# Optimization experiments

Measured on AMD Instinct MI355X. Metric: run time of the kernel, lower is better.

The kernel has to match this reference:

```python
import jax, jax.numpy as jnp
import numpy as np

B, D, R = 256, 4096, 8
MAX_R = 2 * R - 1  # static upper bound on radius (torch uses data-dependent max)


def setup_inputs() -> dict:
    key = jax.random.key(0)
    ks = jax.random.split(key, 6)
    x = jax.random.randint(ks[0], (B, D), 0, 2).astype(jnp.float32)  # binary spins
    W = jax.random.normal(ks[1], (D, D), jnp.float32) / np.float32(np.sqrt(D))
    b = jax.random.normal(ks[2], (D,), jnp.float32)
    radius_raw = jax.random.randint(ks[3], (B, 1), 0, MAX_R)  # +1 in reference -> [1, 2R-1]
    gumbel_u = jax.random.uniform(ks[4], (B, D), jnp.float32)
    u = jax.random.uniform(ks[5], (B,), jnp.float32)
    return {"x": x, "W": W, "b": b, "radius_raw": radius_raw, "gumbel_u": gumbel_u, "u": u}


def _model(x, W, b):
    # quadratic pseudo-Boolean energy model: per-sample scalar score
    return 0.5 * jnp.einsum('bi,ij,bj->b', x, W, x) + x @ b


def reference(x, W, b, radius_raw, gumbel_u, u):
    radius = radius_raw + 1                                   # [B,1] in [1, 2R-1]
    r_mask = (jnp.arange(MAX_R)[None, :] < radius).astype(x.dtype)  # [B, MAX_R]

    score_x = _model(x, W, b)                                 # [B]
    grad = jax.lax.stop_gradient(
        jax.grad(lambda xx: _model(xx, W, b).sum())(x))       # [B,D], detached

    delta_x = -(2.0 * x - 1.0)
    score_change_x = delta_x * grad / 2.0                     # logits of proposal

    # multinomial without replacement == Gumbel top-k on the logits
    eps = 1e-10
    g = -jnp.log(-jnp.log(jnp.clip(gumbel_u, eps, 1.0 - eps)))
    _, indices = jax.lax.top_k(score_change_x + g, MAX_R)     # [B, MAX_R]

    rows = jnp.arange(B)[:, None]
    cur_bits = x[rows, indices]                               # gather
    new_bits = 1.0 - cur_bits
    y = x.at[rows, indices].set(r_mask * new_bits + (1.0 - r_mask) * cur_bits)

    delta_y = -(2.0 * y - 1.0)
    score_y = _model(y, W, b)
    score_change_y = delta_y * grad / 2.0

    log_pypx = score_y - score_x
    log_tilde_pxpy = -jnp.sum(grad * (y - x), axis=-1)
    log_zxzy = (jax.scipy.special.logsumexp(score_change_x, axis=-1)
                - jax.scipy.special.logsumexp(score_change_y, axis=-1))
    log_acc = jnp.minimum(log_pypx + log_tilde_pxpy + log_zxzy, 0.0)

    accepted = (jnp.exp(log_acc) > u).astype(x.dtype)[:, None]  # [B,1]
    return y * accepted + (1.0 - accepted) * x
```

## Files before the change

### kernel.cpp

```cpp
#include <hip/hip_runtime.h>

#define Bsz 256
#define Dd  4096
#define MAXR 15
#define FMAX 3.402823466e+38f
#define BK 64
#define LSTRIDE 72

typedef short bf16x8 __attribute__((ext_vector_type(8)));
typedef float f32x4  __attribute__((ext_vector_type(4)));

__device__ __forceinline__ unsigned short f2bf(float f) {
    unsigned int u = __float_as_uint(f);
    unsigned int r = (u + 0x7fffu + ((u >> 16) & 1u)) >> 16;
    return (unsigned short)r;
}
__device__ __forceinline__ float bf2f(unsigned short h) {
    return __uint_as_float(((unsigned int)h) << 16);
}

__global__ __launch_bounds__(256) void k_ssym(const float* __restrict__ W,
                                              const float* __restrict__ x,
                                              unsigned short* __restrict__ shi,
                                              unsigned short* __restrict__ slo,
                                              unsigned short* __restrict__ xb) {
    __shared__ float t1[64][68];
    __shared__ float t2[64][68];
    int bid = blockIdx.x;
    int bi = 0;
    while (bid >= 64 - bi) { bid -= 64 - bi; ++bi; }
    const int bj = bi + bid;
    const int i0 = bi * 64, j0 = bj * 64;
    const int tid = threadIdx.x;

    #pragma unroll
    for (int sb = 0; sb < 4; ++sb) {
        int s = sb * 256 + tid;
        int r = s >> 4, q = (s & 15) * 4;
        *(float4*)&t1[r][q] = *(const float4*)(W + (size_t)(i0 + r) * Dd + j0 + q);
        *(float4*)&t2[r][q] = *(const float4*)(W + (size_t)(j0 + r) * Dd + i0 + q);
    }
    __syncthreads();

    const int r = tid >> 2, c0 = (tid & 3) * 16;
    {
        unsigned short vh[16], vl[16];
        #pragma unroll
        for (int k = 0; k < 16; ++k) {
            float s = 0.5f * (t1[r][c0 + k] + t2[c0 + k][r]);
            vh[k] = f2bf(s);
            vl[k] = f2bf(s - bf2f(vh[k]));
        }
        size_t o = (size_t)(i0 + r) * Dd + j0 + c0;
        *(uint4*)(shi + o) = *(const uint4*)&vh[0];
        *(uint4*)(shi + o + 8) = *(const uint4*)&vh[8];
        *(uint4*)(slo + o) = *(const uint4*)&vl[0];
        *(uint4*)(slo + o + 8) = *(const uint4*)&vl[8];
    }
    if (bi != bj) {
        unsigned short vh[16], vl[16];
        #pragma unroll
        for (int k = 0; k < 16; ++k) {
            float s = 0.5f * (t2[r][c0 + k] + t1[c0 + k][r]);
            vh[k] = f2bf(s);
            vl[k] = f2bf(s - bf2f(vh[k]));
        }
        size_t o = (size_t)(j0 + r) * Dd + i0 + c0;
        *(uint4*)(shi + o) = *(const uint4*)&vh[0];
        *(uint4*)(shi + o + 8) = *(const uint4*)&vh[8];
        *(uint4*)(slo + o) = *(const uint4*)&vl[0];
        *(uint4*)(slo + o + 8) = *(const uint4*)&vl[8];
    }

    if (blockIdx.x < 256) {
        const float* xp = x + (size_t)blockIdx.x * 4096;
        unsigned short* xo = xb + (size_t)blockIdx.x * 4096;
        #pragma unroll
        for (int c = 0; c < 4; ++c) {
            int e = c * 1024 + tid * 4;
            float4 v = *(const float4*)(xp + e);
            unsigned short o4[4] = { f2bf(v.x), f2bf(v.y), f2bf(v.z), f2bf(v.w) };
            *(uint2*)(xo + e) = *(const uint2*)o4;
        }
    }
}

__global__ __launch_bounds__(128) void k_gemm(const unsigned short* __restrict__ xb,
                                              const unsigned short* __restrict__ shi,
                                              const unsigned short* __restrict__ slo,
                                              float* __restrict__ part,
                                              int kchunk) {
    __shared__ __align__(16) unsigned short As[64 * LSTRIDE];
    __shared__ __align__(16) unsigned short Bh[64 * LSTRIDE];
    __shared__ __align__(16) unsigned short Bl[64 * LSTRIDE];
    const int tid = threadIdx.x;
    const int n0 = blockIdx.x * 64, m0 = blockIdx.y * 64;
    const int kbase = blockIdx.z * kchunk;
    const int w = tid >> 6, lane = tid & 63;
    const int ln = lane & 15, quad = lane >> 4;

    unsigned ga[4], gb[4];
    int lofs[4];
    #pragma unroll
    for (int j = 0; j < 4; ++j) {
        int s = tid + j * 128;
        int r = s >> 3, g = s & 7;
        ga[j]   = (unsigned)((m0 + r) * Dd + kbase + g * 8);
        gb[j]   = (unsigned)((n0 + r) * Dd + kbase + g * 8);
        lofs[j] = r * LSTRIDE + g * 8;
    }

    f32x4 acc[4][2];
    #pragma unroll
    for (int mt = 0; mt < 4; ++mt)
        #pragma unroll
        for (int ct = 0; ct < 2; ++ct)
            #pragma unroll
            for (int rr = 0; rr < 4; ++rr) acc[mt][ct][rr] = 0.0f;

    bf16x8 va[4], vh[4], vl[4];
    #pragma unroll
    for (int j = 0; j < 4; ++j) {
        va[j] = *(const bf16x8*)(xb  + ga[j]);
        vh[j] = *(const bf16x8*)(shi + gb[j]);
        vl[j] = *(const bf16x8*)(slo + gb[j]);
    }

    for (int k0 = 0; k0 < kchunk; k0 += BK) {
        __syncthreads();
        #pragma unroll
        for (int j = 0; j < 4; ++j) {
            *(bf16x8*)&As[lofs[j]] = va[j];
            *(bf16x8*)&Bh[lofs[j]] = vh[j];
            *(bf16x8*)&Bl[lofs[j]] = vl[j];
        }
        {
            int kn = k0 + BK;
            int ks = (kn < kchunk) ? kn : 0;
            #pragma unroll
            for (int j = 0; j < 4; ++j) {
                va[j] = *(const bf16x8*)(xb  + ga[j] + ks);
                vh[j] = *(const bf16x8*)(shi + gb[j] + ks);
                vl[j] = *(const bf16x8*)(slo + gb[j] + ks);
            }
        }
        __syncthreads();
        #pragma unroll
        for (int kk = 0; kk < BK; kk += 32) {
            const int gr = (kk >> 3) + quad;
            bf16x8 a[4];
            #pragma unroll
            for (int mt = 0; mt < 4; ++mt)
                a[mt] = *(const bf16x8*)&As[(mt * 16 + ln) * LSTRIDE + gr * 8];
            #pragma unroll
            for (int ct = 0; ct < 2; ++ct) {
                int rb = w * 32 + ct * 16 + ln;
                bf16x8 bh = *(const bf16x8*)&Bh[rb * LSTRIDE + gr * 8];
                bf16x8 bl = *(const bf16x8*)&Bl[rb * LSTRIDE + gr * 8];
                #pragma unroll
                for (int mt = 0; mt < 4; ++mt) {
                    acc[mt][ct] = __builtin_amdgcn_mfma_f32_16x16x32_bf16(a[mt], bh, acc[mt][ct], 0, 0, 0);
                    acc[mt][ct] = __builtin_amdgcn_mfma_f32_16x16x32_bf16(a[mt], bl, acc[mt][ct], 0, 0, 0);
                }
            }
        }
    }
    float* prow = part + (size_t)blockIdx.z * (Bsz * Dd);
    #pragma unroll
    for (int mt = 0; mt < 4; ++mt)
        #pragma unroll
        for (int ct = 0; ct < 2; ++ct)
            #pragma unroll
            for (int rr = 0; rr < 4; ++rr) {
                int m = m0 + mt * 16 + quad * 4 + rr;
                int n = n0 + w * 32 + ct * 16 + ln;
                prow[(size_t)m * Dd + n] = acc[mt][ct][rr];
            }
}

__device__ __forceinline__ float block_max256(float v, float* redf) {
    #pragma unroll
    for (int off = 32; off; off >>= 1) v = fmaxf(v, __shfl_down(v, off));
    __syncthreads();
    if ((threadIdx.x & 63) == 0) redf[threadIdx.x >> 6] = v;
    __syncthreads();
    return fmaxf(fmaxf(redf[0], redf[1]), fmaxf(redf[2], redf[3]));
}
__device__ __forceinline__ float block_sum256(float v, float* redf) {
    #pragma unroll
    for (int off = 32; off; off >>= 1) v += __shfl_down(v, off);
    __syncthreads();
    if ((threadIdx.x & 63) == 0) redf[threadIdx.x >> 6] = v;
    __syncthreads();
    return (redf[0] + redf[1]) + (redf[2] + redf[3]);
}

__global__ __launch_bounds__(256) void k_epilogue(const float* __restrict__ x,
                                                  const float* __restrict__ W,
                                                  const int* __restrict__ radius_raw,
                                                  const float* __restrict__ gu,
                                                  const float* __restrict__ uvec,
                                                  const float* __restrict__ part,
                                                  const float* __restrict__ bias,
                                                  float* __restrict__ out,
                                                  int nsplit) {
    __shared__ float scx_s[Dd];
    __shared__ float redf[2][4];
    __shared__ int   redi[2][4];
    __shared__ float redsum[4];
    __shared__ int   flips[MAXR];

    const int b = blockIdx.x;
    const int tid = threadIdx.x;
    const float* xrow  = x  + (size_t)b * Dd;
    const float* gurow = gu + (size_t)b * Dd;

    float4 g4[4], bs4[4], xv4[4], uu4[4];
    #pragma unroll
    for (int c = 0; c < 4; ++c) {
        int j = c * 1024 + tid * 4;
        g4[c]  = *(const float4*)(part + (size_t)b * Dd + j);
        bs4[c] = *(const float4*)(bias + j);
        xv4[c] = *(const float4*)(xrow + j);
        uu4[c] = *(const float4*)(gurow + j);
    }
    for (int z = 1; z < nsplit; ++z) {
        const float* pz = part + (size_t)z * (Bsz * Dd) + (size_t)b * Dd;
        #pragma unroll
        for (int c = 0; c < 4; ++c) {
            float4 a = *(const float4*)(pz + c * 1024 + tid * 4);
            g4[c].x += a.x; g4[c].y += a.y; g4[c].z += a.z; g4[c].w += a.w;
        }
    }
    float sc[16], ky[16];
    float lmax = -FMAX;
    float lkey = -FMAX; int lidx = 0x7fffffff;
    #pragma unroll
    for (int c = 0; c < 4; ++c) {
        const float* gg = (const float*)&g4[c];
        const float* gc = (const float*)&bs4[c];
        const float* gx = (const float*)&xv4[c];
        const float* gup = (const float*)&uu4[c];
        #pragma unroll
        for (int e = 0; e < 4; ++e) {
            int r = c * 4 + e;
            float g = gg[e] + gc[e];
            float s = (1.0f - 2.0f * gx[e]) * g * 0.5f;
            float k = s - logf(-logf(fmaxf(gup[e], 1e-10f)));
            sc[r] = s;
            ky[r] = k;
            lmax = fmaxf(lmax, s);
            if (k > lkey) { lkey = k; lidx = c * 1024 + tid * 4 + e; }
        }
        *(float4*)&scx_s[c * 1024 + tid * 4] = *(const float4*)&sc[c * 4];
    }

    float mx = block_max256(lmax, redsum);
    float ls = 0.0f;
    #pragma unroll
    for (int r = 0; r < 16; ++r) ls += expf(sc[r] - mx);
    float sum_x = block_sum256(ls, redsum);
    float lse_x = mx + logf(sum_x);

    const int radius = radius_raw[b] + 1;
    unsigned removed = 0;
    for (int t = 0; t < radius; ++t) {
        float v = lkey; int idx = lidx;
        #pragma unroll
        for (int off = 32; off; off >>= 1) {
            float v2 = __shfl_down(v, off);
            int   i2 = __shfl_down(idx, off);
            if (v2 > v || (v2 == v && i2 < idx)) { v = v2; idx = i2; }
        }
        const int buf = t & 1;
        if ((tid & 63) == 0) { redf[buf][tid >> 6] = v; redi[buf][tid >> 6] = idx; }
        __syncthreads();
        float bv = redf[buf][0]; int bi = redi[buf][0];
        #pragma unroll
        for (int w2 = 1; w2 < 4; ++w2) {
            float v2 = redf[buf][w2]; int i2 = redi[buf][w2];
            if (v2 > bv || (v2 == bv && i2 < bi)) { bv = v2; bi = i2; }
        }
        if (tid == ((bi >> 2) & 255)) {
            removed |= 1u << (((bi >> 10) << 2) | (bi & 3));
            lkey = -FMAX; lidx = 0x7fffffff;
            #pragma unroll
            for (int c = 0; c < 4; ++c)
                #pragma unroll
                for (int e = 0; e < 4; ++e) {
                    int r = c * 4 + e;
                    if (!(removed & (1u << r)) && ky[r] > lkey) {
                        lkey = ky[r]; lidx = c * 1024 + tid * 4 + e;
                    }
                }
        }
        if (tid == 0) flips[t] = bi;
    }
    __syncthreads();

    float delta = 0.0f;
    if (tid < radius) {
        float sv = scx_s[flips[tid]];
        delta = expf(-sv - mx) - expf(sv - mx);
    }
    float sum_y = sum_x + block_sum256(delta, redsum);
    float lse_y = mx + logf(sum_y);

    float ts = 0.0f;
    for (int t = tid; t < radius * radius; t += 256) {
        int p = flips[t / radius], q = flips[t % radius];
        float dp = 1.0f - 2.0f * xrow[p];
        float dq = 1.0f - 2.0f * xrow[q];
        ts += 0.25f * dp * dq * (W[(size_t)p * Dd + q] + W[(size_t)q * Dd + p]);
    }
    float T = block_sum256(ts, redsum);

    float log_acc = fminf(T + lse_x - lse_y, 0.0f);
    int accepted = (expf(log_acc) > uvec[b]) ? 1 : 0;

    float* orow = out + (size_t)b * Dd;
    #pragma unroll
    for (int c = 0; c < 4; ++c)
        *(float4*)(orow + c * 1024 + tid * 4) = xv4[c];
    __syncthreads();
    if (accepted && tid < radius) {
        int p = flips[tid];
        orow[p] = 1.0f - xrow[p];
    }
}

extern "C" void kernel_launch(void* const* d_in, const int* in_sizes, int n_in,
                              void* d_out, int out_size, void* d_ws, size_t ws_size,
                              hipStream_t stream) {
    const float* x          = (const float*)d_in[0];
    const float* W          = (const float*)d_in[1];
    const float* bias       = (const float*)d_in[2];
    const int*   radius_raw = (const int*)d_in[3];
    const float* gu         = (const float*)d_in[4];
    const float* u          = (const float*)d_in[5];
    float* out = (float*)d_out;

    unsigned short* shi = (unsigned short*)d_ws;
    unsigned short* slo = shi + (size_t)Dd * Dd;
    unsigned short* xb  = slo + (size_t)Dd * Dd;
    float*          prt = (float*)(xb + (size_t)Bsz * Dd);

    const size_t fixed = (size_t)2 * Dd * Dd * 2 + (size_t)Bsz * Dd * 2;
    const int nsplit = (ws_size >= fixed + (size_t)4 * Bsz * Dd * 4) ? 4 : 2;
    const int kchunk = Dd / nsplit;

    k_ssym<<<2080, 256, 0, stream>>>(W, x, shi, slo, xb);
    k_gemm<<<dim3(64, 4, nsplit), 128, 0, stream>>>(xb, shi, slo, prt, kchunk);
    k_epilogue<<<Bsz, 256, 0, stream>>>(x, W, radius_raw, gu, u, prt, bias, out, nsplit);
}
```

Measured before the change: 173.4 us.

## Double-buffer GEMM shared tiles and widen epilogue to 512 threads

```diff
diff --git a/kernel.cpp b/kernel.cpp
--- a/kernel.cpp
+++ b/kernel.cpp
@@ -6,6 +6,7 @@
 #define FMAX 3.402823466e+38f
 #define BK 64
 #define LSTRIDE 72
+#define TILE_USH (64 * LSTRIDE)
 
 typedef short bf16x8 __attribute__((ext_vector_type(8)));
 typedef float f32x4  __attribute__((ext_vector_type(4)));
@@ -90,9 +91,9 @@
                                               const unsigned short* __restrict__ slo,
                                               float* __restrict__ part,
                                               int kchunk) {
-    __shared__ __align__(16) unsigned short As[64 * LSTRIDE];
-    __shared__ __align__(16) unsigned short Bh[64 * LSTRIDE];
-    __shared__ __align__(16) unsigned short Bl[64 * LSTRIDE];
+    __shared__ __align__(16) unsigned short As[2 * TILE_USH];
+    __shared__ __align__(16) unsigned short Bh[2 * TILE_USH];
+    __shared__ __align__(16) unsigned short Bl[2 * TILE_USH];
     const int tid = threadIdx.x;
     const int n0 = blockIdx.x * 64, m0 = blockIdx.y * 64;
     const int kbase = blockIdx.z * kchunk;
@@ -126,13 +127,16 @@
         vl[j] = *(const bf16x8*)(slo + gb[j]);
     }
 
-    for (int k0 = 0; k0 < kchunk; k0 += BK) {
-        __syncthreads();
+    int buf = 0;
+    for (int k0 = 0; k0 < kchunk; k0 += BK, buf ^= 1) {
+        unsigned short* Ab = As + buf * TILE_USH;
+        unsigned short* Bhb = Bh + buf * TILE_USH;
+        unsigned short* Blb = Bl + buf * TILE_USH;
         #pragma unroll
         for (int j = 0; j < 4; ++j) {
-            *(bf16x8*)&As[lofs[j]] = va[j];
-            *(bf16x8*)&Bh[lofs[j]] = vh[j];
-            *(bf16x8*)&Bl[lofs[j]] = vl[j];
+            *(bf16x8*)&Ab[lofs[j]]  = va[j];
+            *(bf16x8*)&Bhb[lofs[j]] = vh[j];
+            *(bf16x8*)&Blb[lofs[j]] = vl[j];
         }
         {
             int kn = k0 + BK;
@@ -151,12 +155,12 @@
             bf16x8 a[4];
             #pragma unroll
             for (int mt = 0; mt < 4; ++mt)
-                a[mt] = *(const bf16x8*)&As[(mt * 16 + ln) * LSTRIDE + gr * 8];
+                a[mt] = *(const bf16x8*)&Ab[(mt * 16 + ln) * LSTRIDE + gr * 8];
             #pragma unroll
             for (int ct = 0; ct < 2; ++ct) {
                 int rb = w * 32 + ct * 16 + ln;
-                bf16x8 bh = *(const bf16x8*)&Bh[rb * LSTRIDE + gr * 8];
-                bf16x8 bl = *(const bf16x8*)&Bl[rb * LSTRIDE + gr * 8];
+                bf16x8 bh = *(const bf16x8*)&Bhb[rb * LSTRIDE + gr * 8];
+                bf16x8 bl = *(const bf16x8*)&Blb[rb * LSTRIDE + gr * 8];
                 #pragma unroll
                 for (int mt = 0; mt < 4; ++mt) {
                     acc[mt][ct] = __builtin_amdgcn_mfma_f32_16x16x32_bf16(a[mt], bh, acc[mt][ct], 0, 0, 0);
@@ -178,24 +182,27 @@
             }
 }
 
-__device__ __forceinline__ float block_max256(float v, float* redf) {
+__device__ __forceinline__ float block_max512(float v, float* redf) {
     #pragma unroll
     for (int off = 32; off; off >>= 1) v = fmaxf(v, __shfl_down(v, off));
     __syncthreads();
     if ((threadIdx.x & 63) == 0) redf[threadIdx.x >> 6] = v;
     __syncthreads();
-    return fmaxf(fmaxf(redf[0], redf[1]), fmaxf(redf[2], redf[3]));
-}
-__device__ __forceinline__ float block_sum256(float v, float* redf) {
+    float m01 = fmaxf(redf[0], redf[1]), m23 = fmaxf(redf[2], redf[3]);
+    float m45 = fmaxf(redf[4], redf[5]), m67 = fmaxf(redf[6], redf[7]);
+    return fmaxf(fmaxf(m01, m23), fmaxf(m45, m67));
+}
+__device__ __forceinline__ float block_sum512(float v, float* redf) {
     #pragma unroll
     for (int off = 32; off; off >>= 1) v += __shfl_down(v, off);
     __syncthreads();
     if ((threadIdx.x & 63) == 0) redf[threadIdx.x >> 6] = v;
     __syncthreads();
-    return (redf[0] + redf[1]) + (redf[2] + redf[3]);
-}
-
-__global__ __launch_bounds__(256) void k_epilogue(const float* __restrict__ x,
+    return ((redf[0] + redf[1]) + (redf[2] + redf[3]))
+         + ((redf[4] + redf[5]) + (redf[6] + redf[7]));
+}
+
+__global__ __launch_bounds__(512) void k_epilogue(const float* __restrict__ x,
                                                   const float* __restrict__ W,
                                                   const int* __restrict__ radius_raw,
                                                   const float* __restrict__ gu,
@@ -205,9 +212,9 @@
                                                   float* __restrict__ out,
                                                   int nsplit) {
     __shared__ float scx_s[Dd];
-    __shared__ float redf[2][4];
-    __shared__ int   redi[2][4];
-    __shared__ float redsum[4];
+    __shared__ float redf[2][8];
+    __shared__ int   redi[2][8];
+    __shared__ float redsum[8];
     __shared__ int   flips[MAXR];
 
     const int b = blockIdx.x;
@@ -215,10 +222,10 @@
     const float* xrow  = x  + (size_t)b * Dd;
     const float* gurow = gu + (size_t)b * Dd;
 
-    float4 g4[4], bs4[4], xv4[4], uu4[4];
-    #pragma unroll
-    for (int c = 0; c < 4; ++c) {
-        int j = c * 1024 + tid * 4;
+    float4 g4[2], bs4[2], xv4[2], uu4[2];
+    #pragma unroll
+    for (int c = 0; c < 2; ++c) {
+        int j = c * 2048 + tid * 4;
         g4[c]  = *(const float4*)(part + (size_t)b * Dd + j);
         bs4[c] = *(const float4*)(bias + j);
         xv4[c] = *(const float4*)(xrow + j);
@@ -227,16 +234,16 @@
     for (int z = 1; z < nsplit; ++z) {
         const float* pz = part + (size_t)z * (Bsz * Dd) + (size_t)b * Dd;
         #pragma unroll
-        for (int c = 0; c < 4; ++c) {
-            float4 a = *(const float4*)(pz + c * 1024 + tid * 4);
+        for (int c = 0; c < 2; ++c) {
+            float4 a = *(const float4*)(pz + c * 2048 + tid * 4);
             g4[c].x += a.x; g4[c].y += a.y; g4[c].z += a.z; g4[c].w += a.w;
         }
     }
-    float sc[16], ky[16];
+    float sc[8], ky[8];
     float lmax = -FMAX;
     float lkey = -FMAX; int lidx = 0x7fffffff;
     #pragma unroll
-    for (int c = 0; c < 4; ++c) {
+    for (int c = 0; c < 2; ++c) {
         const float* gg = (const float*)&g4[c];
         const float* gc = (const float*)&bs4[c];
         const float* gx = (const float*)&xv4[c];
@@ -250,16 +257,16 @@
             sc[r] = s;
             ky[r] = k;
             lmax = fmaxf(lmax, s);
-            if (k > lkey) { lkey = k; lidx = c * 1024 + tid * 4 + e; }
-        }
-        *(float4*)&scx_s[c * 1024 + tid * 4] = *(const float4*)&sc[c * 4];
-    }
-
-    float mx = block_max256(lmax, redsum);
+            if (k > lkey) { lkey = k; lidx = c * 2048 + tid * 4 + e; }
+        }
+        *(float4*)&scx_s[c * 2048 + tid * 4] = *(const float4*)&sc[c * 4];
+    }
+
+    float mx = block_max512(lmax, redsum);
     float ls = 0.0f;
     #pragma unroll
-    for (int r = 0; r < 16; ++r) ls += expf(sc[r] - mx);
-    float sum_x = block_sum256(ls, redsum);
+    for (int r = 0; r < 8; ++r) ls += expf(sc[r] - mx);
+    float sum_x = block_sum512(ls, redsum);
     float lse_x = mx + logf(sum_x);
 
     const int radius = radius_raw[b] + 1;
@@ -272,25 +279,25 @@
             int   i2 = __shfl_down(idx, off);
             if (v2 > v || (v2 == v && i2 < idx)) { v = v2; idx = i2; }
         }
-        const int buf = t & 1;
-        if ((tid & 63) == 0) { redf[buf][tid >> 6] = v; redi[buf][tid >> 6] = idx; }
+        const int bsel = t & 1;
+        if ((tid & 63) == 0) { redf[bsel][tid >> 6] = v; redi[bsel][tid >> 6] = idx; }
         __syncthreads();
-        float bv = redf[buf][0]; int bi = redi[buf][0];
-        #pragma unroll
-        for (int w2 = 1; w2 < 4; ++w2) {
-            float v2 = redf[buf][w2]; int i2 = redi[buf][w2];
+        float bv = redf[bsel][0]; int bi = redi[bsel][0];
+        #pragma unroll
+        for (int w2 = 1; w2 < 8; ++w2) {
+            float v2 = redf[bsel][w2]; int i2 = redi[bsel][w2];
             if (v2 > bv || (v2 == bv && i2 < bi)) { bv = v2; bi = i2; }
         }
-        if (tid == ((bi >> 2) & 255)) {
-            removed |= 1u << (((bi >> 10) << 2) | (bi & 3));
+        if (tid == ((bi >> 2) & 511)) {
+            removed |= 1u << (((bi >> 11) << 2) | (bi & 3));
             lkey = -FMAX; lidx = 0x7fffffff;
             #pragma unroll
-            for (int c = 0; c < 4; ++c)
+            for (int c = 0; c < 2; ++c)
                 #pragma unroll
                 for (int e = 0; e < 4; ++e) {
                     int r = c * 4 + e;
                     if (!(removed & (1u << r)) && ky[r] > lkey) {
-                        lkey = ky[r]; lidx = c * 1024 + tid * 4 + e;
+                        lkey = ky[r]; lidx = c * 2048 + tid * 4 + e;
                     }
                 }
         }
@@ -303,25 +310,25 @@
         float sv = scx_s[flips[tid]];
         delta = expf(-sv - mx) - expf(sv - mx);
     }
-    float sum_y = sum_x + block_sum256(delta, redsum);
+    float sum_y = sum_x + block_sum512(delta, redsum);
     float lse_y = mx + logf(sum_y);
 
     float ts = 0.0f;
-    for (int t = tid; t < radius * radius; t += 256) {
+    for (int t = tid; t < radius * radius; t += 512) {
         int p = flips[t / radius], q = flips[t % radius];
         float dp = 1.0f - 2.0f * xrow[p];
         float dq = 1.0f - 2.0f * xrow[q];
         ts += 0.25f * dp * dq * (W[(size_t)p * Dd + q] + W[(size_t)q * Dd + p]);
     }
-    float T = block_sum256(ts, redsum);
+    float T = block_sum512(ts, redsum);
 
     float log_acc = fminf(T + lse_x - lse_y, 0.0f);
     int accepted = (expf(log_acc) > uvec[b]) ? 1 : 0;
 
     float* orow = out + (size_t)b * Dd;
     #pragma unroll
-    for (int c = 0; c < 4; ++c)
-        *(float4*)(orow + c * 1024 + tid * 4) = xv4[c];
+    for (int c = 0; c < 2; ++c)
+        *(float4*)(orow + c * 2048 + tid * 4) = xv4[c];
     __syncthreads();
     if (accepted && tid < radius) {
         int p = flips[tid];
@@ -351,5 +358,5 @@
 
     k_ssym<<<2080, 256, 0, stream>>>(W, x, shi, slo, xb);
     k_gemm<<<dim3(64, 4, nsplit), 128, 0, stream>>>(xb, shi, slo, prt, kchunk);
-    k_epilogue<<<Bsz, 256, 0, stream>>>(x, W, radius_raw, gu, u, prt, bias, out, nsplit);
-}
+    k_epilogue<<<Bsz, 512, 0, stream>>>(x, W, radius_raw, gu, u, prt, bias, out, nsplit);
+}
```

New measurement: 181.1 us. 1.04x slower.

## Split epilogue into parallel elementwise phase and single-wave top-k phase

Applied to the files above, without the earlier changes.

```diff
diff --git a/kernel.cpp b/kernel.cpp
--- a/kernel.cpp
+++ b/kernel.cpp
@@ -178,154 +178,165 @@
             }
 }
 
-__device__ __forceinline__ float block_max256(float v, float* redf) {
-    #pragma unroll
-    for (int off = 32; off; off >>= 1) v = fmaxf(v, __shfl_down(v, off));
+__global__ __launch_bounds__(256) void k_phase1(const float* __restrict__ x,
+                                                const float* __restrict__ gu,
+                                                const float* __restrict__ part,
+                                                const float* __restrict__ bias,
+                                                float* __restrict__ out,
+                                                float* __restrict__ key_ws,
+                                                float* __restrict__ sc_ws,
+                                                float* __restrict__ kmax_ws,
+                                                int*   __restrict__ kidx_ws,
+                                                float* __restrict__ smax_ws,
+                                                float* __restrict__ ssum_ws,
+                                                int nsplit) {
+    const int b = blockIdx.x >> 2, qd = blockIdx.x & 3;
+    const int tid = threadIdx.x;
+    const int j0 = qd * 1024 + tid * 4;
+    const size_t row = (size_t)b * Dd;
+
+    float4 g4 = *(const float4*)(part + row + j0);
+    if (nsplit == 4) {
+        float4 p1 = *(const float4*)(part + (size_t)(1 * Bsz + b) * Dd + j0);
+        float4 p2 = *(const float4*)(part + (size_t)(2 * Bsz + b) * Dd + j0);
+        float4 p3 = *(const float4*)(part + (size_t)(3 * Bsz + b) * Dd + j0);
+        g4.x = ((g4.x + p1.x) + p2.x) + p3.x;
+        g4.y = ((g4.y + p1.y) + p2.y) + p3.y;
+        g4.z = ((g4.z + p1.z) + p2.z) + p3.z;
+        g4.w = ((g4.w + p1.w) + p2.w) + p3.w;
+    } else {
+        for (int z = 1; z < nsplit; ++z) {
+            float4 a = *(const float4*)(part + (size_t)(z * Bsz + b) * Dd + j0);
+            g4.x += a.x; g4.y += a.y; g4.z += a.z; g4.w += a.w;
+        }
+    }
+    float4 bs = *(const float4*)(bias + j0);
+    float4 xv = *(const float4*)(x + row + j0);
+    float4 uu = *(const float4*)(gu + row + j0);
+
+    float sc[4], ky[4];
+    const float* gg = (const float*)&g4;
+    const float* gb = (const float*)&bs;
+    const float* gx = (const float*)&xv;
+    const float* gp = (const float*)&uu;
+    #pragma unroll
+    for (int e = 0; e < 4; ++e) {
+        float g = gg[e] + gb[e];
+        float s = (1.0f - 2.0f * gx[e]) * g * 0.5f;
+        sc[e] = s;
+        ky[e] = s - logf(-logf(fmaxf(gp[e], 1e-10f)));
+    }
+    *(float4*)(sc_ws + row + j0)  = *(const float4*)sc;
+    *(float4*)(key_ws + row + j0) = *(const float4*)ky;
+    *(float4*)(out + row + j0)    = xv;
+
+    float kv = ky[0]; int ki = j0;
+    #pragma unroll
+    for (int e = 1; e < 4; ++e) if (ky[e] > kv) { kv = ky[e]; ki = j0 + e; }
+    #pragma unroll
+    for (int off = 1; off < 16; off <<= 1) {
+        float v2 = __shfl_xor(kv, off); int i2 = __shfl_xor(ki, off);
+        if (v2 > kv || (v2 == kv && i2 < ki)) { kv = v2; ki = i2; }
+    }
+    float sm = fmaxf(fmaxf(sc[0], sc[1]), fmaxf(sc[2], sc[3]));
+    #pragma unroll
+    for (int off = 1; off < 16; off <<= 1) sm = fmaxf(sm, __shfl_xor(sm, off));
+    float es = ((expf(sc[0] - sm) + expf(sc[1] - sm)) + expf(sc[2] - sm)) + expf(sc[3] - sm);
+    #pragma unroll
+    for (int off = 1; off < 16; off <<= 1) es += __shfl_xor(es, off);
+
+    if ((tid & 15) == 0) {
+        int cg = b * 64 + qd * 16 + (tid >> 4);
+        kmax_ws[cg] = kv; kidx_ws[cg] = ki; smax_ws[cg] = sm; ssum_ws[cg] = es;
+    }
+}
+
+__global__ __launch_bounds__(64) void k_phase2(const float* __restrict__ x,
+                                               const float* __restrict__ W,
+                                               const int* __restrict__ radius_raw,
+                                               const float* __restrict__ uvec,
+                                               const float* __restrict__ key_ws,
+                                               const float* __restrict__ sc_ws,
+                                               const float* __restrict__ kmax_ws,
+                                               const int* __restrict__ kidx_ws,
+                                               const float* __restrict__ smax_ws,
+                                               const float* __restrict__ ssum_ws,
+                                               float* __restrict__ out) {
+    __shared__ int   flips[MAXR];
+    __shared__ float xflip[MAXR];
+    const int b = blockIdx.x, lane = threadIdx.x;
+    const size_t row = (size_t)b * Dd;
+
+    float ckmax = kmax_ws[b * 64 + lane];
+    int   ckidx = kidx_ws[b * 64 + lane];
+    float csmax = smax_ws[b * 64 + lane];
+    float cssum = ssum_ws[b * 64 + lane];
+
+    float mx = csmax;
+    #pragma unroll
+    for (int off = 1; off < 64; off <<= 1) mx = fmaxf(mx, __shfl_xor(mx, off));
+    float sum_x = cssum * expf(csmax - mx);
+    #pragma unroll
+    for (int off = 1; off < 64; off <<= 1) sum_x += __shfl_xor(sum_x, off);
+    float lse_x = mx + logf(sum_x);
+
+    const int radius = radius_raw[b] + 1;
+    unsigned rm_lo = 0, rm_hi = 0;
+    const float* keyrow = key_ws + row;
+
+    for (int t = 0; t < radius; ++t) {
+        float v = ckmax; int i = ckidx;
+        #pragma unroll
+        for (int off = 1; off < 64; off <<= 1) {
+            float v2 = __shfl_xor(v, off); int i2 = __shfl_xor(i, off);
+            if (v2 > v || (v2 == v && i2 < i)) { v = v2; i = i2; }
+        }
+        const int bi = i, cw = bi >> 6;
+        if (lane == 0) flips[t] = bi;
+        unsigned lo = __shfl((int)rm_lo, cw), hi = __shfl((int)rm_hi, cw);
+        const int bbit = bi & 63;
+        if (bbit < 32) lo |= 1u << bbit; else hi |= 1u << (bbit - 32);
+        float kv2 = keyrow[cw * 64 + lane];
+        int   id2 = cw * 64 + lane;
+        bool rem = (lane < 32) ? ((lo >> lane) & 1u) : ((hi >> (lane - 32)) & 1u);
+        if (rem) kv2 = -FMAX;
+        #pragma unroll
+        for (int off = 1; off < 64; off <<= 1) {
+            float v2 = __shfl_xor(kv2, off); int i2 = __shfl_xor(id2, off);
+            if (v2 > kv2 || (v2 == kv2 && i2 < id2)) { kv2 = v2; id2 = i2; }
+        }
+        if (lane == cw) { rm_lo = lo; rm_hi = hi; ckmax = kv2; ckidx = id2; }
+    }
     __syncthreads();
-    if ((threadIdx.x & 63) == 0) redf[threadIdx.x >> 6] = v;
+
+    float delta = 0.0f;
+    if (lane < radius) {
+        int p = flips[lane];
+        float sv = sc_ws[row + p];
+        delta = expf(-sv - mx) - expf(sv - mx);
+        xflip[lane] = x[row + p];
+    }
     __syncthreads();
-    return fmaxf(fmaxf(redf[0], redf[1]), fmaxf(redf[2], redf[3]));
-}
-__device__ __forceinline__ float block_sum256(float v, float* redf) {
-    #pragma unroll
-    for (int off = 32; off; off >>= 1) v += __shfl_down(v, off);
-    __syncthreads();
-    if ((threadIdx.x & 63) == 0) redf[threadIdx.x >> 6] = v;
-    __syncthreads();
-    return (redf[0] + redf[1]) + (redf[2] + redf[3]);
-}
-
-__global__ __launch_bounds__(256) void k_epilogue(const float* __restrict__ x,
-                                                  const float* __restrict__ W,
-                                                  const int* __restrict__ radius_raw,
-                                                  const float* __restrict__ gu,
-                                                  const float* __restrict__ uvec,
-                                                  const float* __restrict__ part,
-                                                  const float* __restrict__ bias,
-                                                  float* __restrict__ out,
-                                                  int nsplit) {
-    __shared__ float scx_s[Dd];
-    __shared__ float redf[2][4];
-    __shared__ int   redi[2][4];
-    __shared__ float redsum[4];
-    __shared__ int   flips[MAXR];
-
-    const int b = blockIdx.x;
-    const int tid = threadIdx.x;
-    const float* xrow  = x  + (size_t)b * Dd;
-    const float* gurow = gu + (size_t)b * Dd;
-
-    float4 g4[4], bs4[4], xv4[4], uu4[4];
-    #pragma unroll
-    for (int c = 0; c < 4; ++c) {
-        int j = c * 1024 + tid * 4;
-        g4[c]  = *(const float4*)(part + (size_t)b * Dd + j);
-        bs4[c] = *(const float4*)(bias + j);
-        xv4[c] = *(const float4*)(xrow + j);
-        uu4[c] = *(const float4*)(gurow + j);
-    }
-    for (int z = 1; z < nsplit; ++z) {
-        const float* pz = part + (size_t)z * (Bsz * Dd) + (size_t)b * Dd;
-        #pragma unroll
-        for (int c = 0; c < 4; ++c) {
-            float4 a = *(const float4*)(pz + c * 1024 + tid * 4);
-            g4[c].x += a.x; g4[c].y += a.y; g4[c].z += a.z; g4[c].w += a.w;
-        }
-    }
-    float sc[16], ky[16];
-    float lmax = -FMAX;
-    float lkey = -FMAX; int lidx = 0x7fffffff;
-    #pragma unroll
-    for (int c = 0; c < 4; ++c) {
-        const float* gg = (const float*)&g4[c];
-        const float* gc = (const float*)&bs4[c];
-        const float* gx = (const float*)&xv4[c];
-        const float* gup = (const float*)&uu4[c];
-        #pragma unroll
-        for (int e = 0; e < 4; ++e) {
-            int r = c * 4 + e;
-            float g = gg[e] + gc[e];
-            float s = (1.0f - 2.0f * gx[e]) * g * 0.5f;
-            float k = s - logf(-logf(fmaxf(gup[e], 1e-10f)));
-            sc[r] = s;
-            ky[r] = k;
-            lmax = fmaxf(lmax, s);
-            if (k > lkey) { lkey = k; lidx = c * 1024 + tid * 4 + e; }
-        }
-        *(float4*)&scx_s[c * 1024 + tid * 4] = *(const float4*)&sc[c * 4];
-    }
-
-    float mx = block_max256(lmax, redsum);
-    float ls = 0.0f;
-    #pragma unroll
-    for (int r = 0; r < 16; ++r) ls += expf(sc[r] - mx);
-    float sum_x = block_sum256(ls, redsum);
-    float lse_x = mx + logf(sum_x);
-
-    const int radius = radius_raw[b] + 1;
-    unsigned removed = 0;
-    for (int t = 0; t < radius; ++t) {
-        float v = lkey; int idx = lidx;
-        #pragma unroll
-        for (int off = 32; off; off >>= 1) {
-            float v2 = __shfl_down(v, off);
-            int   i2 = __shfl_down(idx, off);
-            if (v2 > v || (v2 == v && i2 < idx)) { v = v2; idx = i2; }
-        }
-        const int buf = t & 1;
-        if ((tid & 63) == 0) { redf[buf][tid >> 6] = v; redi[buf][tid >> 6] = idx; }
-        __syncthreads();
-        float bv = redf[buf][0]; int bi = redi[buf][0];
-        #pragma unroll
-        for (int w2 = 1; w2 < 4; ++w2) {
-            float v2 = redf[buf][w2]; int i2 = redi[buf][w2];
-            if (v2 > bv || (v2 == bv && i2 < bi)) { bv = v2; bi = i2; }
-        }
-        if (tid == ((bi >> 2) & 255)) {
-            removed |= 1u << (((bi >> 10) << 2) | (bi & 3));
-            lkey = -FMAX; lidx = 0x7fffffff;
-            #pragma unroll
-            for (int c = 0; c < 4; ++c)
-                #pragma unroll
-                for (int e = 0; e < 4; ++e) {
-                    int r = c * 4 + e;
-                    if (!(removed & (1u << r)) && ky[r] > lkey) {
-                        lkey = ky[r]; lidx = c * 1024 + tid * 4 + e;
-                    }
-                }
-        }
-        if (tid == 0) flips[t] = bi;
-    }
-    __syncthreads();
-
-    float delta = 0.0f;
-    if (tid < radius) {
-        float sv = scx_s[flips[tid]];
-        delta = expf(-sv - mx) - expf(sv - mx);
-    }
-    float sum_y = sum_x + block_sum256(delta, redsum);
-    float lse_y = mx + logf(sum_y);
+    float dsum = delta;
+    #pragma unroll
+    for (int off = 1; off < 64; off <<= 1) dsum += __shfl_xor(dsum, off);
+    float lse_y = mx + logf(sum_x + dsum);
 
     float ts = 0.0f;
-    for (int t = tid; t < radius * radius; t += 256) {
+    for (int t = lane; t < radius * radius; t += 64) {
         int p = flips[t / radius], q = flips[t % radius];
-        float dp = 1.0f - 2.0f * xrow[p];
-        float dq = 1.0f - 2.0f * xrow[q];
+        float dp = 1.0f - 2.0f * xflip[t / radius];
+        float dq = 1.0f - 2.0f * xflip[t % radius];
         ts += 0.25f * dp * dq * (W[(size_t)p * Dd + q] + W[(size_t)q * Dd + p]);
     }
-    float T = block_sum256(ts, redsum);
-
-    float log_acc = fminf(T + lse_x - lse_y, 0.0f);
+    #pragma unroll
+    for (int off = 1; off < 64; off <<= 1) ts += __shfl_xor(ts, off);
+
+    float log_acc = fminf(ts + lse_x - lse_y, 0.0f);
     int accepted = (expf(log_acc) > uvec[b]) ? 1 : 0;
-
-    float* orow = out + (size_t)b * Dd;
-    #pragma unroll
-    for (int c = 0; c < 4; ++c)
-        *(float4*)(orow + c * 1024 + tid * 4) = xv4[c];
-    __syncthreads();
-    if (accepted && tid < radius) {
-        int p = flips[tid];
-        orow[p] = 1.0f - xrow[p];
+    if (accepted && lane < radius) {
+        int p = flips[lane];
+        out[row + p] = 1.0f - xflip[lane];
     }
 }
 
@@ -343,13 +354,25 @@
     unsigned short* shi = (unsigned short*)d_ws;
     unsigned short* slo = shi + (size_t)Dd * Dd;
     unsigned short* xb  = slo + (size_t)Dd * Dd;
-    float*          prt = (float*)(xb + (size_t)Bsz * Dd);
+    float* prt = (float*)(xb + (size_t)Bsz * Dd);
 
     const size_t fixed = (size_t)2 * Dd * Dd * 2 + (size_t)Bsz * Dd * 2;
-    const int nsplit = (ws_size >= fixed + (size_t)4 * Bsz * Dd * 4) ? 4 : 2;
+    const size_t per_split = (size_t)Bsz * Dd * 4;
+    const size_t extra = 2 * per_split + 4 * ((size_t)Bsz * 64 * 4);
+    const int nsplit = (ws_size >= fixed + 4 * per_split + extra) ? 4 : 2;
     const int kchunk = Dd / nsplit;
+
+    float* key_ws  = prt + (size_t)nsplit * Bsz * Dd;
+    float* sc_ws   = key_ws + (size_t)Bsz * Dd;
+    float* kmax_ws = sc_ws + (size_t)Bsz * Dd;
+    int*   kidx_ws = (int*)(kmax_ws + Bsz * 64);
+    float* smax_ws = (float*)(kidx_ws + Bsz * 64);
+    float* ssum_ws = smax_ws + Bsz * 64;
 
     k_ssym<<<2080, 256, 0, stream>>>(W, x, shi, slo, xb);
     k_gemm<<<dim3(64, 4, nsplit), 128, 0, stream>>>(xb, shi, slo, prt, kchunk);
-    k_epilogue<<<Bsz, 256, 0, stream>>>(x, W, radius_raw, gu, u, prt, bias, out, nsplit);
-}
+    k_phase1<<<Bsz * 4, 256, 0, stream>>>(x, gu, prt, bias, out, key_ws, sc_ws,
+                                          kmax_ws, kidx_ws, smax_ws, ssum_ws, nsplit);
+    k_phase2<<<Bsz, 64, 0, stream>>>(x, W, radius_raw, u, key_ws, sc_ws,
+                                     kmax_ws, kidx_ws, smax_ws, ssum_ws, out);
+}
```

Result: slower. 179.0 us (+3.3%).

## Split epilogue into wide elementwise phase and per-row top-k selection kernel

Applied to the files above, without the earlier changes.

```diff
diff --git a/kernel.cpp b/kernel.cpp
--- a/kernel.cpp
+++ b/kernel.cpp
@@ -195,71 +195,100 @@
     return (redf[0] + redf[1]) + (redf[2] + redf[3]);
 }
 
-__global__ __launch_bounds__(256) void k_epilogue(const float* __restrict__ x,
-                                                  const float* __restrict__ W,
-                                                  const int* __restrict__ radius_raw,
-                                                  const float* __restrict__ gu,
-                                                  const float* __restrict__ uvec,
-                                                  const float* __restrict__ part,
-                                                  const float* __restrict__ bias,
-                                                  float* __restrict__ out,
-                                                  int nsplit) {
-    __shared__ float scx_s[Dd];
+__global__ __launch_bounds__(256) void k_phase1(const float* __restrict__ x,
+                                                const float* __restrict__ gu,
+                                                const float* __restrict__ part,
+                                                const float* __restrict__ bias,
+                                                float* __restrict__ out,
+                                                float* __restrict__ key_ws,
+                                                float* __restrict__ sc_ws,
+                                                float* __restrict__ lsem_ws,
+                                                float* __restrict__ lses_ws,
+                                                int nsplit) {
+    __shared__ float redf[4];
+    const int b = blockIdx.x >> 2, qd = blockIdx.x & 3;
+    const int tid = threadIdx.x;
+    const int j0 = qd * 1024 + tid * 4;
+    const size_t row = (size_t)b * Dd;
+
+    float4 g4 = *(const float4*)(part + row + j0);
+    if (nsplit == 4) {
+        float4 p1 = *(const float4*)(part + (size_t)(1 * Bsz + b) * Dd + j0);
+        float4 p2 = *(const float4*)(part + (size_t)(2 * Bsz + b) * Dd + j0);
+        float4 p3 = *(const float4*)(part + (size_t)(3 * Bsz + b) * Dd + j0);
+        g4.x = ((g4.x + p1.x) + p2.x) + p3.x;
+        g4.y = ((g4.y + p1.y) + p2.y) + p3.y;
+        g4.z = ((g4.z + p1.z) + p2.z) + p3.z;
+        g4.w = ((g4.w + p1.w) + p2.w) + p3.w;
+    } else {
+        for (int z = 1; z < nsplit; ++z) {
+            float4 a = *(const float4*)(part + (size_t)(z * Bsz + b) * Dd + j0);
+            g4.x += a.x; g4.y += a.y; g4.z += a.z; g4.w += a.w;
+        }
+    }
+    float4 bs = *(const float4*)(bias + j0);
+    float4 xv = *(const float4*)(x + row + j0);
+    float4 uu = *(const float4*)(gu + row + j0);
+
+    float sc[4], ky[4];
+    const float* gg = (const float*)&g4;
+    const float* gb = (const float*)&bs;
+    const float* gx = (const float*)&xv;
+    const float* gp = (const float*)&uu;
+    #pragma unroll
+    for (int e = 0; e < 4; ++e) {
+        float g = gg[e] + gb[e];
+        float s = (1.0f - 2.0f * gx[e]) * g * 0.5f;
+        sc[e] = s;
+        ky[e] = s - logf(-logf(fmaxf(gp[e], 1e-10f)));
+    }
+    *(float4*)(sc_ws + row + j0)  = *(const float4*)sc;
+    *(float4*)(key_ws + row + j0) = *(const float4*)ky;
+    *(float4*)(out + row + j0)    = xv;
+
+    float lm = fmaxf(fmaxf(sc[0], sc[1]), fmaxf(sc[2], sc[3]));
+    lm = block_max256(lm, redf);
+    float es = ((expf(sc[0] - lm) + expf(sc[1] - lm)) + expf(sc[2] - lm)) + expf(sc[3] - lm);
+    es = block_sum256(es, redf);
+    if (tid == 0) { lsem_ws[b * 4 + qd] = lm; lses_ws[b * 4 + qd] = es; }
+}
+
+__global__ __launch_bounds__(256) void k_select(const float* __restrict__ x,
+                                                const float* __restrict__ W,
+                                                const int* __restrict__ radius_raw,
+                                                const float* __restrict__ uvec,
+                                                const float* __restrict__ key_ws,
+                                                const float* __restrict__ sc_ws,
+                                                const float* __restrict__ lsem_ws,
+                                                const float* __restrict__ lses_ws,
+                                                float* __restrict__ out) {
     __shared__ float redf[2][4];
     __shared__ int   redi[2][4];
-    __shared__ float redsum[4];
     __shared__ int   flips[MAXR];
-
     const int b = blockIdx.x;
     const int tid = threadIdx.x;
-    const float* xrow  = x  + (size_t)b * Dd;
-    const float* gurow = gu + (size_t)b * Dd;
-
-    float4 g4[4], bs4[4], xv4[4], uu4[4];
-    #pragma unroll
-    for (int c = 0; c < 4; ++c) {
-        int j = c * 1024 + tid * 4;
-        g4[c]  = *(const float4*)(part + (size_t)b * Dd + j);
-        bs4[c] = *(const float4*)(bias + j);
-        xv4[c] = *(const float4*)(xrow + j);
-        uu4[c] = *(const float4*)(gurow + j);
-    }
-    for (int z = 1; z < nsplit; ++z) {
-        const float* pz = part + (size_t)z * (Bsz * Dd) + (size_t)b * Dd;
-        #pragma unroll
-        for (int c = 0; c < 4; ++c) {
-            float4 a = *(const float4*)(pz + c * 1024 + tid * 4);
-            g4[c].x += a.x; g4[c].y += a.y; g4[c].z += a.z; g4[c].w += a.w;
-        }
-    }
-    float sc[16], ky[16];
-    float lmax = -FMAX;
+    const size_t row = (size_t)b * Dd;
+
+    float ky[16];
+    #pragma unroll
+    for (int c = 0; c < 4; ++c)
+        *(float4*)&ky[c * 4] = *(const float4*)(key_ws + row + c * 1024 + tid * 4);
     float lkey = -FMAX; int lidx = 0x7fffffff;
     #pragma unroll
-    for (int c = 0; c < 4; ++c) {
-        const float* gg = (const float*)&g4[c];
-        const float* gc = (const float*)&bs4[c];
-        const float* gx = (const float*)&xv4[c];
-        const float* gup = (const float*)&uu4[c];
+    for (int c = 0; c < 4; ++c)
         #pragma unroll
         for (int e = 0; e < 4; ++e) {
             int r = c * 4 + e;
-            float g = gg[e] + gc[e];
-            float s = (1.0f - 2.0f * gx[e]) * g * 0.5f;
-            float k = s - logf(-logf(fmaxf(gup[e], 1e-10f)));
-            sc[r] = s;
-            ky[r] = k;
-            lmax = fmaxf(lmax, s);
-            if (k > lkey) { lkey = k; lidx = c * 1024 + tid * 4 + e; }
-        }
-        *(float4*)&scx_s[c * 1024 + tid * 4] = *(const float4*)&sc[c * 4];
-    }
-
-    float mx = block_max256(lmax, redsum);
-    float ls = 0.0f;
-    #pragma unroll
-    for (int r = 0; r < 16; ++r) ls += expf(sc[r] - mx);
-    float sum_x = block_sum256(ls, redsum);
+            if (ky[r] > lkey) { lkey = ky[r]; lidx = c * 1024 + tid * 4 + e; }
+        }
+
+    float m0 = lsem_ws[b * 4 + 0], m1 = lsem_ws[b * 4 + 1];
+    float m2 = lsem_ws[b * 4 + 2], m3 = lsem_ws[b * 4 + 3];
+    float mx = fmaxf(fmaxf(m0, m1), fmaxf(m2, m3));
+    float sum_x = ((lses_ws[b * 4 + 0] * expf(m0 - mx)
+                  + lses_ws[b * 4 + 1] * expf(m1 - mx))
+                  + lses_ws[b * 4 + 2] * expf(m2 - mx))
+                  + lses_ws[b * 4 + 3] * expf(m3 - mx);
     float lse_x = mx + logf(sum_x);
 
     const int radius = radius_raw[b] + 1;
@@ -299,33 +328,30 @@
     __syncthreads();
 
     float delta = 0.0f;
+    float xf = 0.0f;
     if (tid < radius) {
-        float sv = scx_s[flips[tid]];
+        int p = flips[tid];
+        float sv = sc_ws[row + p];
         delta = expf(-sv - mx) - expf(sv - mx);
-    }
-    float sum_y = sum_x + block_sum256(delta, redsum);
+        xf = x[row + p];
+    }
+    float sum_y = sum_x + block_sum256(delta, redf[0]);
     float lse_y = mx + logf(sum_y);
 
     float ts = 0.0f;
     for (int t = tid; t < radius * radius; t += 256) {
         int p = flips[t / radius], q = flips[t % radius];
-        float dp = 1.0f - 2.0f * xrow[p];
-        float dq = 1.0f - 2.0f * xrow[q];
+        float dp = 1.0f - 2.0f * x[row + p];
+        float dq = 1.0f - 2.0f * x[row + q];
         ts += 0.25f * dp * dq * (W[(size_t)p * Dd + q] + W[(size_t)q * Dd + p]);
     }
-    float T = block_sum256(ts, redsum);
+    float T = block_sum256(ts, redf[0]);
 
     float log_acc = fminf(T + lse_x - lse_y, 0.0f);
     int accepted = (expf(log_acc) > uvec[b]) ? 1 : 0;
-
-    float* orow = out + (size_t)b * Dd;
-    #pragma unroll
-    for (int c = 0; c < 4; ++c)
-        *(float4*)(orow + c * 1024 + tid * 4) = xv4[c];
-    __syncthreads();
     if (accepted && tid < radius) {
         int p = flips[tid];
-        orow[p] = 1.0f - xrow[p];
+        out[row + p] = 1.0f - xf;
     }
 }
 
@@ -343,13 +369,23 @@
     unsigned short* shi = (unsigned short*)d_ws;
     unsigned short* slo = shi + (size_t)Dd * Dd;
     unsigned short* xb  = slo + (size_t)Dd * Dd;
-    float*          prt = (float*)(xb + (size_t)Bsz * Dd);
+    float* prt = (float*)(xb + (size_t)Bsz * Dd);
 
     const size_t fixed = (size_t)2 * Dd * Dd * 2 + (size_t)Bsz * Dd * 2;
-    const int nsplit = (ws_size >= fixed + (size_t)4 * Bsz * Dd * 4) ? 4 : 2;
+    const size_t per_split = (size_t)Bsz * Dd * 4;
+    const size_t extra = 2 * per_split + 2 * ((size_t)Bsz * 4 * 4);
+    const int nsplit = (ws_size >= fixed + 4 * per_split + extra) ? 4 : 2;
     const int kchunk = Dd / nsplit;
+
+    float* key_ws  = prt + (size_t)nsplit * Bsz * Dd;
+    float* sc_ws   = key_ws + (size_t)Bsz * Dd;
+    float* lsem_ws = sc_ws + (size_t)Bsz * Dd;
+    float* lses_ws = lsem_ws + Bsz * 4;
 
     k_ssym<<<2080, 256, 0, stream>>>(W, x, shi, slo, xb);
     k_gemm<<<dim3(64, 4, nsplit), 128, 0, stream>>>(xb, shi, slo, prt, kchunk);
-    k_epilogue<<<Bsz, 256, 0, stream>>>(x, W, radius_raw, gu, u, prt, bias, out, nsplit);
-}
+    k_phase1<<<Bsz * 4, 256, 0, stream>>>(x, gu, prt, bias, out, key_ws, sc_ws,
+                                          lsem_ws, lses_ws, nsplit);
+    k_select<<<Bsz, 256, 0, stream>>>(x, W, radius_raw, u, key_ws, sc_ws,
+                                      lsem_ws, lses_ws, out);
+}
```

Result: no change. 175.5 us (+1.2%).
